# Performance work log

Hardware: AMD Instinct MI355X
Metric: run time of the kernel (lower is better)

## Reference

```python
import jax, jax.numpy as jnp
import numpy as np
import math

S, E, D, H = 4096, 512, 64, 8  # sentence_length, imbd_size, hidden_size, num_heads


def setup_inputs() -> dict:
    key = jax.random.key(0)
    k1, k2, k3, k4, k5 = jax.random.split(key, 5)
    return {
        "X": jax.random.normal(k1, (S, E), dtype=jnp.float32),
        "W_q": jax.random.uniform(k2, (H, E, D), dtype=jnp.float32),
        "W_k": jax.random.uniform(k3, (H, E, D), dtype=jnp.float32),
        "W_v": jax.random.uniform(k4, (H, E, D), dtype=jnp.float32),
        "W_0": jax.random.uniform(k5, (E, D), dtype=jnp.float32),
    }


def reference(X, W_q, W_k, W_v, W_0):
    # Per-head projections: X [S,E] broadcast across heads -> [H,S,D]
    q = jnp.einsum('se,hed->hsd', X, W_q)
    k = jnp.einsum('se,hed->hsd', X, W_k)
    v = jnp.einsum('se,hed->hsd', X, W_v)
    # Scaled scores [H,S,S]; softmax over keys (last axis), no mask
    scores = jnp.einsum('hsd,htd->hst', q, k) / math.sqrt(D)
    attn = jax.nn.softmax(scores, axis=-1)
    r3 = jnp.einsum('hst,htd->hsd', attn, v)  # [H,S,D]
    # Concat heads: permute to [S,H,D] -> [S,H*D], then output proj [E,D]
    Z = r3.transpose(1, 0, 2).reshape(S, H * D) @ W_0  # [S,D]
    return Z
```

## Files before the change

### kernel.cpp

```cpp
#include <hip/hip_runtime.h>
#include <hip/hip_bf16.h>

#define S_LEN 4096
#define E_DIM 512
#define D_DIM 64
#define H_NUM 8
#define KSPLIT 4
#define NKT ((S_LEN / KSPLIT) / 64)
#define QSCALE 0.18033688011112042f

typedef short bf16x8 __attribute__((ext_vector_type(8)));
typedef float f32x4 __attribute__((ext_vector_type(4)));
typedef unsigned short u16x8 __attribute__((ext_vector_type(8)));
typedef unsigned short u16x4 __attribute__((ext_vector_type(4)));

__device__ inline unsigned short f2bf(float x) {
    union { float f; unsigned u; } v; v.f = x;
    unsigned r = v.u + 0x7FFFu + ((v.u >> 16) & 1u);
    return (unsigned short)(r >> 16);
}
__device__ inline float bf2f(unsigned short b) {
    union { unsigned u; float f; } v; v.u = ((unsigned)b) << 16;
    return v.f;
}
__device__ inline f32x4 mfma16(bf16x8 a, bf16x8 b, f32x4 c) {
    return __builtin_amdgcn_mfma_f32_16x16x32_bf16(a, b, c, 0, 0, 0);
}
__device__ inline void gl_lds16(const void* g, void* l) {
    __builtin_amdgcn_global_load_lds(
        (const __attribute__((address_space(1))) void*)g,
        (__attribute__((address_space(3))) void*)l, 16, 0, 0);
}

__global__ __launch_bounds__(256) void prepass_x(
    const float* __restrict__ X, unsigned short* __restrict__ Xhi,
    unsigned short* __restrict__ Xlo)
{
    int i = (blockIdx.x * 256 + threadIdx.x) * 4;
    float4 v = *(const float4*)&X[i];
    float a[4] = {v.x, v.y, v.z, v.w};
    u16x4 hv, lv;
#pragma unroll
    for (int j = 0; j < 4; ++j) {
        unsigned short hb = f2bf(a[j]);
        hv[j] = hb;
        lv[j] = f2bf(a[j] - bf2f(hb));
    }
    *(u16x4*)&Xhi[i] = hv;
    *(u16x4*)&Xlo[i] = lv;
}

__global__ __launch_bounds__(256) void prepass_w(
    const float* __restrict__ Wq, const float* __restrict__ Wk,
    const float* __restrict__ Wv, unsigned short* __restrict__ WT)
{
    int z = blockIdx.y;
    const float* W = (z == 0) ? Wq : (z == 1) ? Wk : Wv;
    int idx = blockIdx.x * 256 + threadIdx.x;
    int n = idx >> 7;
    int e = (idx & 127) * 4;
    int hh = n >> 6, d = n & 63;
    unsigned short* Whi = WT + (size_t)z * 2 * 262144;
    unsigned short* Wlo = Whi + 262144;
    u16x4 hv, lv;
#pragma unroll
    for (int j = 0; j < 4; ++j) {
        float v = W[((size_t)hh * E_DIM + e + j) * D_DIM + d];
        unsigned short hb = f2bf(v);
        hv[j] = hb;
        lv[j] = f2bf(v - bf2f(hb));
    }
    *(u16x4*)&Whi[(size_t)n * E_DIM + e] = hv;
    *(u16x4*)&Wlo[(size_t)n * E_DIM + e] = lv;
}

__global__ __launch_bounds__(256) void proj_kernel(
    const unsigned short* __restrict__ Xhi, const unsigned short* __restrict__ Xlo,
    const unsigned short* __restrict__ WT,
    unsigned short* __restrict__ Qhi, unsigned short* __restrict__ Qlo,
    unsigned short* __restrict__ Khi, unsigned short* __restrict__ Klo,
    unsigned short* __restrict__ Vb)
{
    __shared__ __align__(16) unsigned short XhS[128 * 64];
    __shared__ __align__(16) unsigned short XlS[128 * 64];
    __shared__ __align__(16) unsigned short WhS[128 * 64];
    __shared__ __align__(16) unsigned short WlS[128 * 64];

    const int s0 = blockIdx.x * 128, n0 = blockIdx.y * 128, z = blockIdx.z;
    const unsigned short* Wh_g = WT + (size_t)z * 524288;
    const unsigned short* Wl_g = Wh_g + 262144;

    const int tid = threadIdx.x, lane = tid & 63, w = tid >> 6;
    const int l15 = lane & 15, lhi = lane >> 4;
    const int wr = w >> 1, wc = w & 1;

    const int chunk = lane & 7;
    size_t aoff[4], boff[4];
    int ldso[4];
#pragma unroll
    for (int i = 0; i < 4; ++i) {
        int r = w * 32 + i * 8 + (lane >> 3);
        int swz = (chunk * 16) ^ ((r & 7) << 4);
        aoff[i] = ((size_t)(s0 + r)) * 1024 + swz;
        boff[i] = ((size_t)(n0 + r)) * 1024 + swz;
        ldso[i] = (w * 32 + i * 8) * 128;
    }

    f32x4 acc[4][4];
#pragma unroll
    for (int a = 0; a < 4; ++a)
#pragma unroll
        for (int b = 0; b < 4; ++b) acc[a][b] = (f32x4){0.f, 0.f, 0.f, 0.f};

    for (int kb = 0; kb < E_DIM; kb += 64) {
        __syncthreads();
#pragma unroll
        for (int i = 0; i < 4; ++i) {
            size_t ab = aoff[i] + kb * 2;
            size_t bb = boff[i] + kb * 2;
            gl_lds16((const char*)Xhi + ab, (char*)XhS + ldso[i]);
            gl_lds16((const char*)Xlo + ab, (char*)XlS + ldso[i]);
            gl_lds16((const char*)Wh_g + bb, (char*)WhS + ldso[i]);
            gl_lds16((const char*)Wl_g + bb, (char*)WlS + ldso[i]);
        }
        __syncthreads();

#pragma unroll
        for (int kc = 0; kc < 2; ++kc) {
            int cb = kc * 64 + lhi * 16;
            bf16x8 ah[4], al[4], bh[4], bl[4];
#pragma unroll
            for (int rt = 0; rt < 4; ++rt) {
                int row = wr * 64 + rt * 16 + l15;
                int ad = row * 128 + (cb ^ ((row & 7) << 4));
                ah[rt] = *(const bf16x8*)((const char*)XhS + ad);
                al[rt] = *(const bf16x8*)((const char*)XlS + ad);
            }
#pragma unroll
            for (int nt = 0; nt < 4; ++nt) {
                int n = wc * 64 + nt * 16 + l15;
                int bd = n * 128 + (cb ^ ((n & 7) << 4));
                bh[nt] = *(const bf16x8*)((const char*)WhS + bd);
                bl[nt] = *(const bf16x8*)((const char*)WlS + bd);
            }
#pragma unroll
            for (int rt = 0; rt < 4; ++rt)
#pragma unroll
                for (int nt = 0; nt < 4; ++nt) {
                    acc[rt][nt] = mfma16(ah[rt], bh[nt], acc[rt][nt]);
                    acc[rt][nt] = mfma16(ah[rt], bl[nt], acc[rt][nt]);
                    acc[rt][nt] = mfma16(al[rt], bh[nt], acc[rt][nt]);
                }
        }
    }

#pragma unroll
    for (int rt = 0; rt < 4; ++rt)
#pragma unroll
        for (int nt = 0; nt < 4; ++nt) {
            int n = n0 + wc * 64 + nt * 16 + l15;
            int hh = n >> 6, d = n & 63;
#pragma unroll
            for (int j = 0; j < 4; ++j) {
                int s = s0 + wr * 64 + rt * 16 + lhi * 4 + j;
                float val = acc[rt][nt][j];
                size_t o = ((size_t)hh * S_LEN + s) * D_DIM + d;
                if (z == 0) {
                    val *= QSCALE;
                    unsigned short hb = f2bf(val);
                    Qhi[o] = hb;
                    Qlo[o] = f2bf(val - bf2f(hb));
                } else if (z == 1) {
                    unsigned short hb = f2bf(val);
                    Khi[o] = hb;
                    Klo[o] = f2bf(val - bf2f(hb));
                } else {
                    Vb[o] = f2bf(val);
                }
            }
        }
}

__global__ __launch_bounds__(256) void pack_vt(
    const unsigned short* __restrict__ Vb, unsigned short* __restrict__ Vt)
{
    __shared__ unsigned short T[64][72];
    int h = blockIdx.y, sblk = blockIdx.x * 64;
    int t = threadIdx.x;
#pragma unroll
    for (int p = 0; p < 2; ++p) {
        int slot = t + 256 * p;
        int s = slot >> 3, c = slot & 7;
        u16x8 v = *(const u16x8*)&Vb[((size_t)h * S_LEN + sblk + s) * D_DIM + c * 8];
#pragma unroll
        for (int j = 0; j < 8; ++j) T[c * 8 + j][s] = v[j];
    }
    __syncthreads();
#pragma unroll
    for (int p = 0; p < 2; ++p) {
        int slot = t + 256 * p;
        int d = slot >> 3, c = slot & 7;
        u16x8 v;
#pragma unroll
        for (int j = 0; j < 8; ++j) v[j] = T[d][c * 8 + j];
        *(u16x8*)&Vt[((size_t)(h * D_DIM + d)) * S_LEN + sblk + c * 8] = v;
    }
}

__global__ __launch_bounds__(256) void flash_kernel(
    const unsigned short* __restrict__ Qhi, const unsigned short* __restrict__ Qlo,
    const unsigned short* __restrict__ Khi_g, const unsigned short* __restrict__ Klo_g,
    const unsigned short* __restrict__ Vt_g,
    unsigned short* __restrict__ Part, float2* __restrict__ ML)
{
    __shared__ __align__(16) unsigned short KhiS[64 * 64];
    __shared__ __align__(16) unsigned short KloS[64 * 64];
    __shared__ __align__(16) unsigned short VtS[64 * 64];
    __shared__ __align__(16) unsigned short PS[4][16 * 64];

    const int h  = blockIdx.y;
    const int ks = blockIdx.z;
    const int q0 = blockIdx.x * 64;
    const int tid  = threadIdx.x;
    const int lane = tid & 63;
    const int w    = tid >> 6;
    const int l15  = lane & 15;
    const int lhi  = lane >> 4;

    const int qrow = q0 + w * 16 + l15;
    bf16x8 qh[2], ql[2];
#pragma unroll
    for (int c = 0; c < 2; ++c) {
        size_t off = ((size_t)(h * S_LEN + qrow)) * D_DIM + lhi * 8 + 32 * c;
        qh[c] = *(const bf16x8*)&Qhi[off];
        ql[c] = *(const bf16x8*)&Qlo[off];
    }

    const char *pKh[2], *pKl[2], *pV[2];
    int ldsd[2];
    {
        const int chunk = lane & 7;
#pragma unroll
        for (int i = 0; i < 2; ++i) {
            int r = w * 16 + i * 8 + (lane >> 3);
            int swz = (chunk * 16) ^ ((r & 7) << 4);
            size_t kb = ((size_t)(h * S_LEN + ks * (S_LEN / KSPLIT) + r)) * 128 + swz;
            pKh[i] = (const char*)Khi_g + kb;
            pKl[i] = (const char*)Klo_g + kb;
            size_t vb = ((size_t)(h * D_DIM + r) * S_LEN + ks * (S_LEN / KSPLIT)) * 2 + swz;
            pV[i] = (const char*)Vt_g + vb;
            ldsd[i] = (w * 16 + i * 8) * 128;
        }
    }

    f32x4 acc_o[4];
#pragma unroll
    for (int nt = 0; nt < 4; ++nt) acc_o[nt] = (f32x4){0.f, 0.f, 0.f, 0.f};
    float m2[4], l[4];
#pragma unroll
    for (int r = 0; r < 4; ++r) { m2[r] = -1e30f; l[r] = 0.f; }

    for (int kt = 0; kt < NKT; ++kt) {
        __syncthreads();
#pragma unroll
        for (int i = 0; i < 2; ++i) {
            gl_lds16(pKh[i], (char*)KhiS + ldsd[i]);
            gl_lds16(pKl[i], (char*)KloS + ldsd[i]);
            gl_lds16(pV[i],  (char*)VtS  + ldsd[i]);
            pKh[i] += 8192; pKl[i] += 8192; pV[i] += 128;
        }
        __syncthreads();

        f32x4 sacc[4];
#pragma unroll
        for (int nt = 0; nt < 4; ++nt) sacc[nt] = (f32x4){0.f, 0.f, 0.f, 0.f};
#pragma unroll
        for (int c = 0; c < 2; ++c) {
            int colb = (lhi * 8 + 32 * c) * 2;
#pragma unroll
            for (int nt = 0; nt < 4; ++nt) {
                int key = l15 + 16 * nt;
                int lo = key * 128 + (((colb >> 4) ^ (key & 7)) << 4);
                bf16x8 kh = *(const bf16x8*)((const char*)KhiS + lo);
                bf16x8 kl = *(const bf16x8*)((const char*)KloS + lo);
                sacc[nt] = mfma16(qh[c], kh, sacc[nt]);
                sacc[nt] = mfma16(qh[c], kl, sacc[nt]);
                sacc[nt] = mfma16(ql[c], kh, sacc[nt]);
            }
        }

        float p[4][4];
#pragma unroll
        for (int r = 0; r < 4; ++r) {
            float vm = fmaxf(fmaxf(sacc[0][r], sacc[1][r]), fmaxf(sacc[2][r], sacc[3][r]));
#pragma unroll
            for (int off = 1; off < 16; off <<= 1) vm = fmaxf(vm, __shfl_xor(vm, off));
            if (vm > m2[r] + 8.f) {
                float sc = exp2f(m2[r] - vm);
                m2[r] = vm;
                l[r] *= sc;
#pragma unroll
                for (int nt = 0; nt < 4; ++nt) acc_o[nt][r] *= sc;
            }
            float sum = 0.f;
#pragma unroll
            for (int nt = 0; nt < 4; ++nt) {
                float pv = exp2f(sacc[nt][r] - m2[r]);
                p[nt][r] = pv;
                sum += pv;
            }
#pragma unroll
            for (int off = 1; off < 16; off <<= 1) sum += __shfl_xor(sum, off);
            l[r] += sum;
        }

        unsigned short* pw = &PS[w][0];
#pragma unroll
        for (int nt = 0; nt < 4; ++nt) {
            int colb = (l15 + 16 * nt) * 2;
#pragma unroll
            for (int r = 0; r < 4; ++r) {
                int row = lhi * 4 + r;
                int lo = row * 128 + (((colb >> 4) ^ (row & 7)) << 4) + (colb & 15);
                *(unsigned short*)((char*)pw + lo) = f2bf(p[nt][r]);
            }
        }

#pragma unroll
        for (int c = 0; c < 2; ++c) {
            int colb = (lhi * 8 + 32 * c) * 2;
            int loA = l15 * 128 + (((colb >> 4) ^ (l15 & 7)) << 4);
            bf16x8 pa = *(const bf16x8*)((const char*)pw + loA);
#pragma unroll
            for (int nt = 0; nt < 4; ++nt) {
                int d = l15 + 16 * nt;
                int loB = d * 128 + (((colb >> 4) ^ (d & 7)) << 4);
                bf16x8 vb = *(const bf16x8*)((const char*)VtS + loB);
                acc_o[nt] = mfma16(pa, vb, acc_o[nt]);
            }
        }
    }

    unsigned short* PT = Part + ((size_t)(ks * H_NUM + h)) * S_LEN * D_DIM;
#pragma unroll
    for (int r = 0; r < 4; ++r) {
        float inv = 1.f / l[r];
        int s = q0 + w * 16 + lhi * 4 + r;
#pragma unroll
        for (int nt = 0; nt < 4; ++nt)
            PT[(size_t)s * D_DIM + l15 + 16 * nt] = f2bf(acc_o[nt][r] * inv);
        if (l15 == 0)
            ML[(size_t)(ks * H_NUM + h) * S_LEN + s] = make_float2(m2[r], l[r]);
    }
}

__global__ __launch_bounds__(256) void cw_kernel(
    const float2* __restrict__ ML, float4* __restrict__ CW)
{
    int i = blockIdx.x * 256 + threadIdx.x;
    float2 a[KSPLIT];
    float m = -1e30f;
#pragma unroll
    for (int k = 0; k < KSPLIT; ++k) {
        a[k] = ML[(size_t)k * H_NUM * S_LEN + i];
        m = fmaxf(m, a[k].x);
    }
    float wk[KSPLIT], wsum = 0.f;
#pragma unroll
    for (int k = 0; k < KSPLIT; ++k) {
        wk[k] = exp2f(a[k].x - m) * a[k].y;
        wsum += wk[k];
    }
    float inv = 1.f / wsum;
    CW[i] = make_float4(wk[0] * inv, wk[1] * inv, wk[2] * inv, wk[3] * inv);
}

__global__ __launch_bounds__(256) void zout_kernel(
    const unsigned short* __restrict__ Part, const float4* __restrict__ CW,
    const float* __restrict__ W0, float* __restrict__ Z)
{
    __shared__ __align__(16) float Rs[32][64];
    __shared__ __align__(16) float Ws[32][64];

    const size_t PSZ = (size_t)H_NUM * S_LEN * D_DIM;
    const int s0 = blockIdx.x * 64;
    const int tid = threadIdx.x;
    const int tx = tid & 15;
    const int ty = tid >> 4;

    float acc[4][4];
#pragma unroll
    for (int i = 0; i < 4; ++i)
#pragma unroll
        for (int j = 0; j < 4; ++j) acc[i][j] = 0.f;

    for (int kb = 0; kb < E_DIM; kb += 32) {
        __syncthreads();
#pragma unroll
        for (int p = 0; p < 2; ++p) {
            int idx = tid + 256 * p;
            int row = idx >> 3;
            int kq  = idx & 7;
            int k = kb + kq * 4;
            int hh = k >> 6, d0 = k & 63;
            int s = s0 + row;
            size_t pbase = ((size_t)hh * S_LEN + s) * D_DIM + d0;
            float4 c = *(const float4*)&CW[hh * S_LEN + s];
            u16x4 a0 = *(const u16x4*)&Part[pbase];
            u16x4 a1 = *(const u16x4*)&Part[PSZ + pbase];
            u16x4 a2 = *(const u16x4*)&Part[2 * PSZ + pbase];
            u16x4 a3 = *(const u16x4*)&Part[3 * PSZ + pbase];
#pragma unroll
            for (int j = 0; j < 4; ++j)
                Rs[kq * 4 + j][row] = bf2f(a0[j]) * c.x + bf2f(a1[j]) * c.y +
                                      bf2f(a2[j]) * c.z + bf2f(a3[j]) * c.w;
        }
#pragma unroll
        for (int p = 0; p < 2; ++p) {
            int idx = tid + 256 * p;
            int k  = idx >> 4;
            int nq = idx & 15;
            *(float4*)&Ws[k][nq * 4] = *(const float4*)&W0[(size_t)(kb + k) * D_DIM + nq * 4];
        }
        __syncthreads();

#pragma unroll 8
        for (int k = 0; k < 32; ++k) {
            float a[4], b[4];
            *(float4*)&a[0] = *(const float4*)&Rs[k][ty * 4];
            *(float4*)&b[0] = *(const float4*)&Ws[k][tx * 4];
#pragma unroll
            for (int i = 0; i < 4; ++i)
#pragma unroll
                for (int j = 0; j < 4; ++j) acc[i][j] += a[i] * b[j];
        }
    }

#pragma unroll
    for (int i = 0; i < 4; ++i) {
        float4 o = make_float4(acc[i][0], acc[i][1], acc[i][2], acc[i][3]);
        *(float4*)&Z[(size_t)(s0 + ty * 4 + i) * D_DIM + tx * 4] = o;
    }
}

extern "C" void kernel_launch(void* const* d_in, const int* in_sizes, int n_in,
                              void* d_out, int out_size, void* d_ws, size_t ws_size,
                              hipStream_t stream) {
    const float* X  = (const float*)d_in[0];
    const float* Wq = (const float*)d_in[1];
    const float* Wk = (const float*)d_in[2];
    const float* Wv = (const float*)d_in[3];
    const float* W0 = (const float*)d_in[4];

    char* ws = (char*)d_ws;
    const size_t MB = 1ull << 20;
    unsigned short* Qhi = (unsigned short*)(ws + 0 * MB);
    unsigned short* Qlo = (unsigned short*)(ws + 4 * MB);
    unsigned short* Khi = (unsigned short*)(ws + 8 * MB);
    unsigned short* Klo = (unsigned short*)(ws + 12 * MB);
    unsigned short* Vt  = (unsigned short*)(ws + 16 * MB);
    unsigned short* Vb  = (unsigned short*)(ws + 20 * MB);
    unsigned short* Xhi = (unsigned short*)(ws + 24 * MB);
    unsigned short* Xlo = (unsigned short*)(ws + 28 * MB);
    unsigned short* WT  = (unsigned short*)(ws + 32 * MB);
    unsigned short* Part = (unsigned short*)(ws + 20 * MB);
    float2* ML = (float2*)(ws + 36 * MB);
    float4* CW = (float4*)(ws + 37 * MB);

    float* Z = (float*)d_out;

    prepass_x<<<dim3(S_LEN * E_DIM / 4 / 256), 256, 0, stream>>>(X, Xhi, Xlo);
    prepass_w<<<dim3(E_DIM * 128 / 256, 3), 256, 0, stream>>>(Wq, Wk, Wv, WT);
    proj_kernel<<<dim3(S_LEN / 128, 4, 3), 256, 0, stream>>>(
        Xhi, Xlo, WT, Qhi, Qlo, Khi, Klo, Vb);
    pack_vt<<<dim3(S_LEN / 64, H_NUM), 256, 0, stream>>>(Vb, Vt);
    flash_kernel<<<dim3(S_LEN / 64, H_NUM, KSPLIT), 256, 0, stream>>>(
        Qhi, Qlo, Khi, Klo, Vt, Part, ML);
    cw_kernel<<<dim3(H_NUM * S_LEN / 256), 256, 0, stream>>>(ML, CW);
    zout_kernel<<<dim3(S_LEN / 64), 256, 0, stream>>>(Part, CW, W0, Z);
}
```

Before: 279.9 us.

## Transpose score MFMA so softmax rows live per lane, pack P stores

Swaps the MFMA operand order for QK^T so each lane holds a single query row's scores across its accumulator elements. The row max and sum now need only two cross-lane shuffles instead of four per row, and the running max and sum shrink to one scalar per lane. The lazy rescale becomes wave-uniform via __all. P is converted with packed v_cvt_pk_bf16_f32 and written as 8-byte stores instead of scalar 16-bit stores. The rescale path now needs shuffles to broadcast scale factors to the output accumulator layout, and the softmax code depends on the transposed register layout being correct.

```diff
diff --git a/kernel.cpp b/kernel.cpp
--- a/kernel.cpp
+++ b/kernel.cpp
@@ -30,6 +30,11 @@
     __builtin_amdgcn_global_load_lds(
         (const __attribute__((address_space(1))) void*)g,
         (__attribute__((address_space(3))) void*)l, 16, 0, 0);
+}
+__device__ inline unsigned cvtpk(float a, float b) {
+    unsigned r;
+    asm volatile("v_cvt_pk_bf16_f32 %0, %1, %2" : "=v"(r) : "v"(a), "v"(b));
+    return r;
 }
 
 __global__ __launch_bounds__(256) void prepass_x(
@@ -256,9 +261,9 @@
     f32x4 acc_o[4];
 #pragma unroll
     for (int nt = 0; nt < 4; ++nt) acc_o[nt] = (f32x4){0.f, 0.f, 0.f, 0.f};
-    float m2[4], l[4];
-#pragma unroll
-    for (int r = 0; r < 4; ++r) { m2[r] = -1e30f; l[r] = 0.f; }
+    float m2 = -1e30f, lsum = 0.f;
+
+    unsigned short* pw = &PS[w][0];
 
     for (int kt = 0; kt < NKT; ++kt) {
         __syncthreads();
@@ -283,48 +288,50 @@
                 int lo = key * 128 + (((colb >> 4) ^ (key & 7)) << 4);
                 bf16x8 kh = *(const bf16x8*)((const char*)KhiS + lo);
                 bf16x8 kl = *(const bf16x8*)((const char*)KloS + lo);
-                sacc[nt] = mfma16(qh[c], kh, sacc[nt]);
-                sacc[nt] = mfma16(qh[c], kl, sacc[nt]);
-                sacc[nt] = mfma16(ql[c], kh, sacc[nt]);
+                sacc[nt] = mfma16(kh, qh[c], sacc[nt]);
+                sacc[nt] = mfma16(kl, qh[c], sacc[nt]);
+                sacc[nt] = mfma16(kh, ql[c], sacc[nt]);
             }
         }
 
-        float p[4][4];
-#pragma unroll
-        for (int r = 0; r < 4; ++r) {
-            float vm = fmaxf(fmaxf(sacc[0][r], sacc[1][r]), fmaxf(sacc[2][r], sacc[3][r]));
-#pragma unroll
-            for (int off = 1; off < 16; off <<= 1) vm = fmaxf(vm, __shfl_xor(vm, off));
-            if (vm > m2[r] + 8.f) {
-                float sc = exp2f(m2[r] - vm);
-                m2[r] = vm;
-                l[r] *= sc;
-#pragma unroll
-                for (int nt = 0; nt < 4; ++nt) acc_o[nt][r] *= sc;
-            }
-            float sum = 0.f;
-#pragma unroll
-            for (int nt = 0; nt < 4; ++nt) {
-                float pv = exp2f(sacc[nt][r] - m2[r]);
-                p[nt][r] = pv;
-                sum += pv;
-            }
-#pragma unroll
-            for (int off = 1; off < 16; off <<= 1) sum += __shfl_xor(sum, off);
-            l[r] += sum;
-        }
-
-        unsigned short* pw = &PS[w][0];
+        float mx0 = fmaxf(fmaxf(sacc[0][0], sacc[0][1]), fmaxf(sacc[0][2], sacc[0][3]));
+        float mx1 = fmaxf(fmaxf(sacc[1][0], sacc[1][1]), fmaxf(sacc[1][2], sacc[1][3]));
+        float mx2 = fmaxf(fmaxf(sacc[2][0], sacc[2][1]), fmaxf(sacc[2][2], sacc[2][3]));
+        float mx3 = fmaxf(fmaxf(sacc[3][0], sacc[3][1]), fmaxf(sacc[3][2], sacc[3][3]));
+        float vm = fmaxf(fmaxf(mx0, mx1), fmaxf(mx2, mx3));
+        vm = fmaxf(vm, __shfl_xor(vm, 16));
+        vm = fmaxf(vm, __shfl_xor(vm, 32));
+
+        if (!__all(vm <= m2 + 8.f)) {
+            float mnew = fmaxf(m2, vm);
+            float sc = exp2f(m2 - mnew);
+            m2 = mnew;
+            lsum *= sc;
+            float scj[4];
+#pragma unroll
+            for (int j = 0; j < 4; ++j) scj[j] = __shfl(sc, lhi * 4 + j);
+#pragma unroll
+            for (int nt = 0; nt < 4; ++nt)
+#pragma unroll
+                for (int j = 0; j < 4; ++j) acc_o[nt][j] *= scj[j];
+        }
+
+        float sum = 0.f;
 #pragma unroll
         for (int nt = 0; nt < 4; ++nt) {
-            int colb = (l15 + 16 * nt) * 2;
-#pragma unroll
-            for (int r = 0; r < 4; ++r) {
-                int row = lhi * 4 + r;
-                int lo = row * 128 + (((colb >> 4) ^ (row & 7)) << 4) + (colb & 15);
-                *(unsigned short*)((char*)pw + lo) = f2bf(p[nt][r]);
-            }
-        }
+            float e0 = exp2f(sacc[nt][0] - m2);
+            float e1 = exp2f(sacc[nt][1] - m2);
+            float e2 = exp2f(sacc[nt][2] - m2);
+            float e3 = exp2f(sacc[nt][3] - m2);
+            sum += (e0 + e1) + (e2 + e3);
+            int colb = 32 * nt + 8 * lhi;
+            int adr = l15 * 128 + ((((colb >> 4)) ^ (l15 & 7)) << 4) + (colb & 15);
+            uint2 pk = make_uint2(cvtpk(e0, e1), cvtpk(e2, e3));
+            *(uint2*)((char*)pw + adr) = pk;
+        }
+        sum += __shfl_xor(sum, 16);
+        sum += __shfl_xor(sum, 32);
+        lsum += sum;
 
 #pragma unroll
         for (int c = 0; c < 2; ++c) {
@@ -341,16 +348,19 @@
         }
     }
 
+    if (lane < 16) {
+        ML[(size_t)(ks * H_NUM + h) * S_LEN + q0 + w * 16 + l15] =
+            make_float2(m2, lsum);
+    }
     unsigned short* PT = Part + ((size_t)(ks * H_NUM + h)) * S_LEN * D_DIM;
 #pragma unroll
     for (int r = 0; r < 4; ++r) {
-        float inv = 1.f / l[r];
+        float lr = __shfl(lsum, lhi * 4 + r);
+        float inv = 1.f / lr;
         int s = q0 + w * 16 + lhi * 4 + r;
 #pragma unroll
         for (int nt = 0; nt < 4; ++nt)
             PT[(size_t)s * D_DIM + l15 + 16 * nt] = f2bf(acc_o[nt][r] * inv);
-        if (l15 == 0)
-            ML[(size_t)(ks * H_NUM + h) * S_LEN + s] = make_float2(m2[r], l[r]);
     }
 }
 
```

Measured after the change: 228.2 us. 1.23x faster.
